# Optimization experiments

Hardware: AMD Instinct MI355X
Metric: run time of the kernel (lower is better)

## Reference

```python
import jax, jax.numpy as jnp
import numpy as np

N = 100000            # number of nodes
E = 1600000           # number of edges (avg degree 16)
D = 32                # embedding dim
MASK_DEPTH = 3        # cfg.mask_depth
PATH_PROB = 0.5       # cfg.path_prob
NUM_MASK_CAND = 1024  # cfg.num_mask_cand
EPS_NORM = 1e-12      # F.normalize eps


def setup_inputs() -> dict:
    key = jax.random.key(0)
    k1, k2 = jax.random.split(key)
    edge_index = jax.random.randint(k1, (2, E), 0, N)  # [2, E] (row, col) COO indices
    adj_values = jnp.ones((E,), dtype=jnp.float32)     # sparse values (binary adjacency)
    embeds = jax.random.normal(k2, (N, D), dtype=jnp.float32)
    return {"edge_index": edge_index, "adj_values": adj_values, "embeds": embeds}


def _spmm(rows, cols, vals, x):
    # out[i] = sum_{e: rows[e]==i} vals[e] * x[cols[e]]  -- irregular gather + scatter-add
    return jax.ops.segment_sum(x[cols] * vals[:, None], rows, num_segments=N)


def _l2_normalize(x):
    n = jnp.sqrt(jnp.sum(x * x, axis=-1, keepdims=True))
    return x / jnp.maximum(n, EPS_NORM)


def reference(edge_index, adj_values, embeds):
    rows, cols = edge_index[0], edge_index[1]
    vals = adj_values

    # order = row-sums of sparse adj, shape [N, 1]
    order = jax.ops.segment_sum(vals, rows, num_segments=N)[:, None]

    fst_emb = _spmm(rows, cols, vals, embeds) - embeds
    fst_num = order
    emb = [fst_emb]
    num = [fst_num]

    drop_key = jax.random.key(42)
    for i in range(MASK_DEPTH):
        # sparse_dropout with keep prob path_prob**(i+1); zeroing values == dropping edges in spmm
        keep_prob = PATH_PROB ** (i + 1)
        u = jax.random.uniform(jax.random.fold_in(drop_key, i), (E,))
        keep = jnp.floor(u + keep_prob)  # 1.0 with prob keep_prob, else 0.0
        vals = vals * keep               # dropout compounds across iterations

        emb.append(_spmm(rows, cols, vals, emb[-1]) - emb[-1] - order * emb[-1])
        num.append(_spmm(rows, cols, vals, num[-1]) - num[-1] - order)
        order = jax.ops.segment_sum(vals, rows, num_segments=N)[:, None]

    subgraph_embeds = sum(emb) / (sum(num) + 1e-8)
    subgraph_embeds = _l2_normalize(subgraph_embeds)
    embeds_n = _l2_normalize(embeds)

    scores = jnp.sum(subgraph_embeds * embeds_n, axis=-1)  # [N]
    # Gumbel noise: -log(-log(U))
    u = jax.random.uniform(jax.random.key(7), (N,))
    scores = scores + (-jnp.log(-jnp.log(u)))

    _, candidates = jax.lax.top_k(scores, NUM_MASK_CAND)
    return scores, candidates
```

## Files before the change

kernel.cpp:

```cpp
#include <hip/hip_runtime.h>
#include <stdint.h>
#include <stddef.h>

#define NN 100000
#define NE 1600000
#define DD 32
#define NCAND 1024
#define HSIZE 65536
#define SORTN 4096
#define NBUK ((NN + 255) / 256)
#define EPB 4096
#define BCAP 5120
#define BCAPL 4608
#define CHK 5

#define CAP1 832000
#define CAP2 432000
#define CAP3 240000

__host__ __device__ inline void tf2x32(uint32_t k0, uint32_t k1, uint32_t x0, uint32_t x1,
                                       uint32_t& o0, uint32_t& o1) {
  uint32_t ks2 = k0 ^ k1 ^ 0x1BD11BDAu;
  uint32_t v0 = x0 + k0, v1 = x1 + k1;
#define TFR(r) { v0 += v1; v1 = (v1 << (r)) | (v1 >> (32 - (r))); v1 ^= v0; }
  TFR(13) TFR(15) TFR(26) TFR(6)   v0 += k1;  v1 += ks2 + 1u;
  TFR(17) TFR(29) TFR(16) TFR(24)  v0 += ks2; v1 += k0 + 2u;
  TFR(13) TFR(15) TFR(26) TFR(6)   v0 += k0;  v1 += k1 + 3u;
  TFR(17) TFR(29) TFR(16) TFR(24)  v0 += k1;  v1 += ks2 + 4u;
  TFR(13) TFR(15) TFR(26) TFR(6)   v0 += ks2; v1 += k0 + 5u;
#undef TFR
  o0 = v0; o1 = v1;
}

__device__ __forceinline__ uint32_t jax_bits32(uint32_t k0, uint32_t k1, uint32_t i) {
  uint32_t o0, o1;
  tf2x32(k0, k1, 0u, i, o0, o1);
  return o0 ^ o1;
}

__device__ __forceinline__ float bits_to_uniform(uint32_t b) {
  return __fsub_rn(__uint_as_float((b >> 9) | 0x3f800000u), 1.0f);
}

__device__ __forceinline__ float pw32c(float4 c0, float4 c1, float4 c2, float4 c3,
                                       float4 c4, float4 c5, float4 c6, float4 c7) {
  float r0 = __fadd_rn(__fadd_rn(__fadd_rn(c0.x, c2.x), c4.x), c6.x);
  float r1 = __fadd_rn(__fadd_rn(__fadd_rn(c0.y, c2.y), c4.y), c6.y);
  float r2 = __fadd_rn(__fadd_rn(__fadd_rn(c0.z, c2.z), c4.z), c6.z);
  float r3 = __fadd_rn(__fadd_rn(__fadd_rn(c0.w, c2.w), c4.w), c6.w);
  float r4 = __fadd_rn(__fadd_rn(__fadd_rn(c1.x, c3.x), c5.x), c7.x);
  float r5 = __fadd_rn(__fadd_rn(__fadd_rn(c1.y, c3.y), c5.y), c7.y);
  float r6 = __fadd_rn(__fadd_rn(__fadd_rn(c1.z, c3.z), c5.z), c7.z);
  float r7 = __fadd_rn(__fadd_rn(__fadd_rn(c1.w, c3.w), c5.w), c7.w);
  float a01 = __fadd_rn(r0, r1), a23 = __fadd_rn(r2, r3);
  float a45 = __fadd_rn(r4, r5), a67 = __fadd_rn(r6, r7);
  return __fadd_rn(__fadd_rn(a01, a23), __fadd_rn(a45, a67));
}

__device__ __forceinline__ float4 f4div1(float4 a, float d) {
  return make_float4(__fdiv_rn(a.x, d), __fdiv_rn(a.y, d),
                     __fdiv_rn(a.z, d), __fdiv_rn(a.w, d));
}
__device__ __forceinline__ float4 f4sq(float4 a) {
  return make_float4(__fmul_rn(a.x, a.x), __fmul_rn(a.y, a.y),
                     __fmul_rn(a.z, a.z), __fmul_rn(a.w, a.w));
}
__device__ __forceinline__ float4 f4dd(float4 s, float n1, float4 e, float n2) {
  return make_float4(__fmul_rn(__fdiv_rn(s.x, n1), __fdiv_rn(e.x, n2)),
                     __fmul_rn(__fdiv_rn(s.y, n1), __fdiv_rn(e.y, n2)),
                     __fmul_rn(__fdiv_rn(s.z, n1), __fdiv_rn(e.z, n2)),
                     __fmul_rn(__fdiv_rn(s.w, n1), __fdiv_rn(e.w, n2)));
}

__global__ __launch_bounds__(1024) void kA2_bin(
    const int* __restrict__ rows, const int* __restrict__ cols,
    const float* __restrict__ adj,
    uint32_t k00, uint32_t k01, uint32_t k10, uint32_t k11,
    uint32_t k20, uint32_t k21,
    int* __restrict__ bucketCursor, int4* __restrict__ pkBin,
    int* __restrict__ bucketCntS) {
  __shared__ int hist[NBUK];
  __shared__ int base[NBUK];
  __shared__ int h1[NBUK];
  __shared__ int h2[NBUK];
  __shared__ int h3[NBUK];
  __shared__ uint8_t lvs[EPB];
  __shared__ uint16_t rank16[EPB];
  int tid = threadIdx.x;
  for (int i = tid; i < NBUK; i += 1024) { hist[i] = 0; h1[i] = 0; h2[i] = 0; h3[i] = 0; }
  __syncthreads();
  int e0 = blockIdx.x * EPB;
#pragma unroll
  for (int k = 0; k < 4; ++k) {
    int e = e0 + k * 1024 + tid;
    int lv = 0;
    if (e < NE) {
      float u0 = bits_to_uniform(jax_bits32(k00, k01, (uint32_t)e));
      float u1 = bits_to_uniform(jax_bits32(k10, k11, (uint32_t)e));
      float u2 = bits_to_uniform(jax_bits32(k20, k21, (uint32_t)e));
      float kp0 = floorf(__fadd_rn(u0, 0.5f));
      float kp1 = floorf(__fadd_rn(u1, 0.25f));
      float kp2 = floorf(__fadd_rn(u2, 0.125f));
      if (kp0 != 0.0f) { lv = 1; if (kp1 != 0.0f) { lv = 2; if (kp2 != 0.0f) lv = 3; } }
      int b = rows[e] >> 8;
      rank16[k * 1024 + tid] = (uint16_t)atomicAdd(&hist[b], 1);
      if (lv >= 1) {
        atomicAdd(&h1[b], 1);
        if (lv >= 2) {
          atomicAdd(&h2[b], 1);
          if (lv >= 3) atomicAdd(&h3[b], 1);
        }
      }
    }
    lvs[k * 1024 + tid] = (uint8_t)lv;
  }
  __syncthreads();
  for (int i = tid; i < NBUK; i += 1024) {
    int h = hist[i];
    base[i] = (h > 0) ? atomicAdd(&bucketCursor[i], h) : 0;
    if (h1[i]) atomicAdd(&bucketCntS[i], h1[i]);
    if (h2[i]) atomicAdd(&bucketCntS[NBUK + i], h2[i]);
    if (h3[i]) atomicAdd(&bucketCntS[2 * NBUK + i], h3[i]);
  }
  __syncthreads();
#pragma unroll
  for (int k = 0; k < 4; ++k) {
    int e = e0 + k * 1024 + tid;
    if (e < NE) {
      int r = rows[e];
      int b = r >> 8;
      int lv = (int)lvs[k * 1024 + tid];
      int pos = base[b] + (int)rank16[k * 1024 + tid];
      if (pos < BCAP)
        pkBin[(size_t)b * BCAP + pos] =
            make_int4(cols[e], __float_as_int(adj[e]), (e << 2) | lv, r);
    }
  }
}

__global__ __launch_bounds__(512) void k_scanBS(const int* __restrict__ bucketCursor,
                                                const int* __restrict__ bucketCntS,
                                                int* __restrict__ bucketBaseS) {
  __shared__ int sb[512];
  int a = blockIdx.x;
  const int* c = (a == 0) ? bucketCursor : (bucketCntS + (size_t)(a - 1) * NBUK);
  int* o = bucketBaseS + (size_t)a * (NBUK + 1);
  int tid = threadIdx.x;
  int v = (tid < NBUK) ? c[tid] : 0;
  sb[tid] = v;
  __syncthreads();
  for (int off = 1; off < 512; off <<= 1) {
    int x = (tid >= off) ? sb[tid - off] : 0;
    __syncthreads();
    sb[tid] += x;
    __syncthreads();
  }
  if (tid < NBUK) o[tid] = sb[tid] - v;
  if (tid == NBUK - 1) o[NBUK] = sb[tid];
}

__global__ __launch_bounds__(1024) void kB_emit(
    const int* __restrict__ bucketBaseS, const int4* __restrict__ pkBin,
    int* __restrict__ rpAll,
    int2* __restrict__ pk0, int2* __restrict__ pk1,
    int2* __restrict__ pk2, int2* __restrict__ pk3,
    float* __restrict__ order0, float* __restrict__ order1, float* __restrict__ order2) {
  __shared__ unsigned long long cnt64[256];
  __shared__ unsigned long long scan64[1024];
  __shared__ int start0[256];
  __shared__ int cur[256];
  __shared__ uint32_t keyF[BCAPL];
  __shared__ uint32_t keyG[BCAPL];
  __shared__ uint16_t origG[BCAPL];
  int b = blockIdx.x, tid = threadIdx.x;
  int bB0 = bucketBaseS[b];
  int n = bucketBaseS[b + 1] - bB0;
  if (n > BCAPL) n = BCAPL;
  size_t sRead = (size_t)b * BCAP;
  const int* pkI = (const int*)pkBin;
  const int2* pkZW = (const int2*)pkBin;
  int r0 = b << 8;
  int nr = NN - r0; if (nr > 256) nr = 256;
  int bB1 = bucketBaseS[(NBUK + 1) + b];
  int bB2 = bucketBaseS[2 * (NBUK + 1) + b];
  int bB3 = bucketBaseS[3 * (NBUK + 1) + b];
  if (tid < 256) { cnt64[tid] = 0ull; cur[tid] = 0; }
  __syncthreads();
  for (int i = tid; i < n; i += 1024) {
    int2 zw = pkZW[2 * (sRead + (size_t)i) + 1];
    int lr = zw.y - r0;
    int lv = zw.x & 3;
    keyF[i] = ((uint32_t)lr << 23) | (uint32_t)zw.x;
    unsigned long long add = 1ull;
    if (lv >= 1) add |= 1ull << 16;
    if (lv >= 2) add |= 1ull << 32;
    if (lv >= 3) add |= 1ull << 48;
    atomicAdd(&cnt64[lr], add);
  }
  __syncthreads();
  unsigned long long own = (tid < 256) ? cnt64[tid] : 0ull;
  if (tid < 256) scan64[tid] = own;
  __syncthreads();
  for (int off = 1; off < 256; off <<= 1) {
    unsigned long long v = (tid < 256 && tid >= off) ? scan64[tid - off] : 0ull;
    __syncthreads();
    if (tid < 256) scan64[tid] += v;
    __syncthreads();
  }
  if (tid < 256) {
    unsigned long long ex = scan64[tid] - own;
    start0[tid] = (int)(ex & 0xFFFFull);
    if (tid < nr) {
      rpAll[r0 + tid] = bB0 + (int)(ex & 0xFFFFull);
      rpAll[(NN + 1) + r0 + tid] = bB1 + (int)((ex >> 16) & 0xFFFFull);
      rpAll[2 * (NN + 1) + r0 + tid] = bB2 + (int)((ex >> 32) & 0xFFFFull);
      rpAll[3 * (NN + 1) + r0 + tid] = bB3 + (int)((ex >> 48) & 0xFFFFull);
    }
  }
  if (b == NBUK - 1 && tid == 0) {
    rpAll[NN] = bucketBaseS[NBUK];
    rpAll[(NN + 1) + NN] = bucketBaseS[(NBUK + 1) + NBUK];
    rpAll[2 * (NN + 1) + NN] = bucketBaseS[2 * (NBUK + 1) + NBUK];
    rpAll[3 * (NN + 1) + NN] = bucketBaseS[3 * (NBUK + 1) + NBUK];
  }
  __syncthreads();
  for (int i = tid; i < n; i += 1024) {
    uint32_t k = keyF[i];
    int lr = (int)(k >> 23);
    int slot = start0[lr] + atomicAdd(&cur[lr], 1);
    origG[slot] = (uint16_t)i;
    keyG[slot] = k;
  }
  __syncthreads();
  int C2 = (n + 1023) >> 10;
  {
    int lo2 = tid * C2, hi2 = lo2 + C2;
    if (lo2 > n) lo2 = n;
    if (hi2 > n) hi2 = n;
    uint16_t vals[CHK];
    uint16_t pos[CHK];
    uint32_t keys[CHK];
#pragma unroll
    for (int q = 0; q < CHK; ++q) {
      int i = lo2 + q;
      if (i < hi2) {
        uint32_t ki = keyG[i];
        int lr = (int)(ki >> 23);
        int st = start0[lr];
        int d = (int)(cnt64[lr] & 0xFFFFull);
        int rank = 0;
        for (int j = 0; j < d; ++j) rank += (keyG[st + j] < ki) ? 1 : 0;
        vals[q] = origG[i];
        keys[q] = ki;
        pos[q] = (uint16_t)(st + rank);
      }
    }
    __syncthreads();
#pragma unroll
    for (int q = 0; q < CHK; ++q) {
      int i = lo2 + q;
      if (i < hi2) { origG[pos[q]] = vals[q]; keyG[pos[q]] = keys[q]; }
    }
  }
  __syncthreads();
  uint32_t* adjS = keyF;
  {
    uint32_t av[CHK];
#pragma unroll
    for (int q = 0; q < CHK; ++q) {
      int i = tid + q * 1024;
      if (i < n) av[q] = (uint32_t)pkI[4 * (sRead + (size_t)origG[i]) + 1];
    }
#pragma unroll
    for (int q = 0; q < CHK; ++q) {
      int i = tid + q * 1024;
      if (i < n) adjS[i] = av[q];
    }
  }
  __syncthreads();
  if (tid < nr) {
    int d = (int)(cnt64[tid] & 0xFFFFull);
    int st = start0[tid];
    float o0 = 0.0f, o1v = 0.0f, o2v = 0.0f;
    for (int i = 0; i < d; ++i) {
      int lv = (int)(keyG[st + i] & 3u);
      float a = __uint_as_float(adjS[st + i]);
      o0 = __fadd_rn(o0, a);
      if (lv >= 1) { o1v = __fadd_rn(o1v, a); if (lv >= 2) o2v = __fadd_rn(o2v, a); }
    }
    order0[r0 + tid] = o0; order1[r0 + tid] = o1v; order2[r0 + tid] = o2v;
  }
  int lo = tid * C2, hi = lo + C2;
  if (lo > n) lo = n;
  if (hi > n) hi = n;
  int c1 = 0, c2 = 0, c3 = 0;
  for (int i = lo; i < hi; ++i) {
    int lv = (int)(keyG[i] & 3u);
    c1 += (lv >= 1); c2 += (lv >= 2); c3 += (lv >= 3);
  }
  unsigned long long mine = (unsigned long long)c1 |
                            ((unsigned long long)c2 << 16) |
                            ((unsigned long long)c3 << 32);
  scan64[tid] = mine;
  __syncthreads();
  for (int off = 1; off < 1024; off <<= 1) {
    unsigned long long v = (tid >= off) ? scan64[tid - off] : 0ull;
    __syncthreads();
    scan64[tid] += v;
    __syncthreads();
  }
  unsigned long long ex = scan64[tid] - mine;
  int o1 = bB1 + (int)(ex & 0xFFFFull);
  int o2 = bB2 + (int)((ex >> 16) & 0xFFFFull);
  int o3 = bB3 + (int)((ex >> 32) & 0xFFFFull);
  {
    int colr[CHK];
#pragma unroll
    for (int q = 0; q < CHK; ++q) {
      int i = lo + q;
      if (i < hi) colr[q] = pkI[4 * (sRead + (size_t)origG[i])];
    }
#pragma unroll
    for (int q = 0; q < CHK; ++q) {
      int i = lo + q;
      if (i < hi) {
        int lv = (int)(keyG[i] & 3u);
        int2 pkv = make_int2(colr[q], (int)adjS[i]);
        pk0[bB0 + i] = pkv;
        if (lv >= 1) {
          pk1[o1++] = pkv;
          if (lv >= 2) {
            pk2[o2++] = pkv;
            if (lv >= 3) pk3[o3++] = pkv;
          }
        }
      }
    }
  }
}


__global__ void k_emb0(const int* __restrict__ rp, const int2* __restrict__ pk,
                       const float* __restrict__ embeds, float* __restrict__ e0) {
  int tid = blockIdx.x * blockDim.x + threadIdx.x;
  int r = tid >> 5, d = tid & 31;
  if (r >= NN) return;
  int s = rp[r], t = rp[r + 1];
  float acc = 0.0f;
  for (int base = s; base < t; base += 32) {
    int idx = base + d;
    int2 p = (idx < t) ? pk[idx] : make_int2(0, 0);
    int m = t - base; if (m > 32) m = 32;
    for (int j = 0; j < m; j += 8) {
      int cc[8], aa[8];
      float xx[8];
#pragma unroll
      for (int q = 0; q < 8; ++q) {
        cc[q] = __shfl(p.x, j + q, 32);
        aa[q] = __shfl(p.y, j + q, 32);
      }
#pragma unroll
      for (int q = 0; q < 8; ++q) xx[q] = embeds[(size_t)cc[q] * DD + d];
#pragma unroll
      for (int q = 0; q < 8; ++q)
        acc = __fadd_rn(acc, __fmul_rn(__int_as_float(aa[q]), xx[q]));
    }
  }
  e0[(size_t)r * DD + d] = __fsub_rn(acc, embeds[(size_t)r * DD + d]);
}

__global__ void k_emb_step(const int* __restrict__ rp, const int2* __restrict__ pk,
                           const float* __restrict__ ord, const float* __restrict__ ecur,
                           float* __restrict__ enext, float* __restrict__ esum,
                           const float* __restrict__ ncur, float* __restrict__ nnext,
                           float* __restrict__ nsum, int mode) {
  int tid = blockIdx.x * blockDim.x + threadIdx.x;
  int r = tid >> 5, d = tid & 31;
  if (r >= NN) return;
  int s = rp[r], t = rp[r + 1];
  float acc = 0.0f, accn = 0.0f;
  for (int base = s; base < t; base += 32) {
    int idx = base + d;
    int2 p = (idx < t) ? pk[idx] : make_int2(0, 0);
    int m = t - base; if (m > 32) m = 32;
    for (int j = 0; j < m; j += 8) {
      int cc[8], aa[8];
      float xx[8], nn[8];
#pragma unroll
      for (int q = 0; q < 8; ++q) {
        cc[q] = __shfl(p.x, j + q, 32);
        aa[q] = __shfl(p.y, j + q, 32);
      }
#pragma unroll
      for (int q = 0; q < 8; ++q) {
        xx[q] = ecur[(size_t)cc[q] * DD + d];
        nn[q] = ncur[cc[q]];
      }
#pragma unroll
      for (int q = 0; q < 8; ++q) {
        float av = __int_as_float(aa[q]);
        acc = __fadd_rn(acc, __fmul_rn(av, xx[q]));
        accn = __fadd_rn(accn, __fmul_rn(av, nn[q]));
      }
    }
  }
  float ordv = ord[r];
  size_t idx = (size_t)r * DD + d;
  float ec = ecur[idx];
  float o = __fsub_rn(__fsub_rn(acc, ec), __fmul_rn(ordv, ec));
  if (mode != 3) enext[idx] = o;
  if (mode == 1) esum[idx] = __fadd_rn(ec, o);
  else esum[idx] = __fadd_rn(esum[idx], o);
  if (d == 0) {
    float nc = ncur[r];
    float on = __fsub_rn(__fsub_rn(accn, nc), ordv);
    if (mode != 3) nnext[r] = on;
    if (mode == 1) nsum[r] = __fadd_rn(nc, on);
    else nsum[r] = __fadd_rn(nsum[r], on);
  }
}

__global__ __launch_bounds__(256) void k_score(
    const float* __restrict__ embeds, const float* __restrict__ emb_sum,
    const float* __restrict__ num_sum, uint32_t gk0, uint32_t gk1,
    float* __restrict__ out_scores) {
  __shared__ float sm[256 * 33];
  int t = threadIdx.x;
  int b = blockIdx.x;
  int f4base = b * 2048;
  const float4* gS = (const float4*)emb_sum;
  const float4* gE = (const float4*)embeds;
#pragma unroll
  for (int k = 0; k < 8; ++k) {
    int loc = k * 256 + t;
    int g = f4base + loc;
    if (g < NN * 8) {
      int row = loc >> 3, c4 = loc & 7;
      float4 v = gS[g];
      float* d1 = &sm[row * 33 + c4 * 4];
      d1[0] = v.x; d1[1] = v.y; d1[2] = v.z; d1[3] = v.w;
    }
  }
  __syncthreads();
  int r = b * 256 + t;
  int rc = (r < NN) ? r : 0;
  float denom = __fadd_rn(num_sum[rc], 1e-8f);
  const float* rs = &sm[t * 33];
  float4 s0 = f4div1(make_float4(rs[0], rs[1], rs[2], rs[3]), denom);
  float4 s1 = f4div1(make_float4(rs[4], rs[5], rs[6], rs[7]), denom);
  float4 s2 = f4div1(make_float4(rs[8], rs[9], rs[10], rs[11]), denom);
  float4 s3 = f4div1(make_float4(rs[12], rs[13], rs[14], rs[15]), denom);
  float4 s4 = f4div1(make_float4(rs[16], rs[17], rs[18], rs[19]), denom);
  float4 s5 = f4div1(make_float4(rs[20], rs[21], rs[22], rs[23]), denom);
  float4 s6 = f4div1(make_float4(rs[24], rs[25], rs[26], rs[27]), denom);
  float4 s7 = f4div1(make_float4(rs[28], rs[29], rs[30], rs[31]), denom);
  float n1 = fmaxf(__fsqrt_rn(pw32c(f4sq(s0), f4sq(s1), f4sq(s2), f4sq(s3),
                                    f4sq(s4), f4sq(s5), f4sq(s6), f4sq(s7))), 1e-12f);
  __syncthreads();
#pragma unroll
  for (int k = 0; k < 8; ++k) {
    int loc = k * 256 + t;
    int g = f4base + loc;
    if (g < NN * 8) {
      int row = loc >> 3, c4 = loc & 7;
      float4 w = gE[g];
      float* d2 = &sm[row * 33 + c4 * 4];
      d2[0] = w.x; d2[1] = w.y; d2[2] = w.z; d2[3] = w.w;
    }
  }
  __syncthreads();
  float4 m0 = make_float4(rs[0], rs[1], rs[2], rs[3]);
  float4 m1 = make_float4(rs[4], rs[5], rs[6], rs[7]);
  float4 m2 = make_float4(rs[8], rs[9], rs[10], rs[11]);
  float4 m3 = make_float4(rs[12], rs[13], rs[14], rs[15]);
  float4 m4 = make_float4(rs[16], rs[17], rs[18], rs[19]);
  float4 m5 = make_float4(rs[20], rs[21], rs[22], rs[23]);
  float4 m6 = make_float4(rs[24], rs[25], rs[26], rs[27]);
  float4 m7 = make_float4(rs[28], rs[29], rs[30], rs[31]);
  float n2 = fmaxf(__fsqrt_rn(pw32c(f4sq(m0), f4sq(m1), f4sq(m2), f4sq(m3),
                                    f4sq(m4), f4sq(m5), f4sq(m6), f4sq(m7))), 1e-12f);
  float dot = pw32c(f4dd(s0, n1, m0, n2), f4dd(s1, n1, m1, n2),
                    f4dd(s2, n1, m2, n2), f4dd(s3, n1, m3, n2),
                    f4dd(s4, n1, m4, n2), f4dd(s5, n1, m5, n2),
                    f4dd(s6, n1, m6, n2), f4dd(s7, n1, m7, n2));
  float u = bits_to_uniform(jax_bits32(gk0, gk1, (uint32_t)rc));
  float l1 = (float)log((double)u);
  float w = -l1;
  float l2 = (float)log((double)w);
  float g = -l2;
  if (r < NN) out_scores[r] = __fadd_rn(dot, g);
}

__global__ __launch_bounds__(1024) void k_hist(const float* __restrict__ scores,
                                               int* __restrict__ hist) {
  __shared__ uint32_t hb[1024];
  __shared__ uint32_t hc[1024];
  int t = threadIdx.x;
  int r = blockIdx.x * 1024 + t;
  hb[t] = 0xFFFFFFFFu;
  hc[t] = 0u;
  __syncthreads();
  if (r < NN) {
    uint32_t kb = __float_as_uint(scores[r]);
    kb = (kb & 0x80000000u) ? ~kb : (kb | 0x80000000u);
    uint32_t key = kb >> 16;
    uint32_t slot = (key * 2654435761u) >> 22;
    for (;;) {
      uint32_t prev = atomicCAS(&hb[slot], 0xFFFFFFFFu, key);
      if (prev == 0xFFFFFFFFu || prev == key) { atomicAdd(&hc[slot], 1u); break; }
      slot = (slot + 1) & 1023u;
    }
  }
  __syncthreads();
  if (hb[t] != 0xFFFFFFFFu) atomicAdd(&hist[hb[t]], (int)hc[t]);
}

__global__ void k_cutoff(const int* __restrict__ hist, int* __restrict__ cutoff) {
  __shared__ int psum[1024];
  int t = threadIdx.x;
  int base = HSIZE - (t + 1) * 64;
  int own = 0;
  for (int i = 0; i < 64; ++i) own += hist[base + i];
  psum[t] = own;
  __syncthreads();
  for (int off = 1; off < 1024; off <<= 1) {
    int v = (t >= off) ? psum[t - off] : 0;
    __syncthreads();
    psum[t] += v;
    __syncthreads();
  }
  int incl = psum[t];
  int prev = incl - own;
  if (incl >= NCAND && prev < NCAND) {
    int c = prev;
    int b = HSIZE - t * 64 - 1;
    while (b >= base) {
      c += hist[b];
      if (c >= NCAND) break;
      --b;
    }
    *cutoff = b;
  }
}

__global__ void k_collect(const float* __restrict__ scores, const int* __restrict__ cutoff,
                          unsigned long long* __restrict__ buf, int* __restrict__ cnt2) {
  int r = blockIdx.x * blockDim.x + threadIdx.x;
  if (r >= NN) return;
  uint32_t kb = __float_as_uint(scores[r]);
  kb = (kb & 0x80000000u) ? ~kb : (kb | 0x80000000u);
  if ((int)(kb >> 16) >= *cutoff) {
    int p = atomicAdd(cnt2, 1);
    if (p < SORTN)
      buf[p] = ((unsigned long long)kb << 32) | (uint32_t)(~(uint32_t)r);
  }
}

__global__ __launch_bounds__(256) void k_rank(const unsigned long long* __restrict__ buf,
                                              const int* __restrict__ cnt2,
                                              float* __restrict__ out_cand) {
  __shared__ unsigned long long s[SORTN];
  int m = *cnt2;
  if (m > SORTN) m = SORTN;
  if (blockIdx.x * 256 >= m) return;
  for (int i = threadIdx.x; i < m; i += 256) s[i] = buf[i];
  __syncthreads();
  int i = blockIdx.x * 256 + threadIdx.x;
  if (i >= m) return;
  unsigned long long mine = s[i];
  int rank = 0;
  int j = 0;
  for (; j + 8 <= m; j += 8) {
#pragma unroll
    for (int q = 0; q < 8; ++q) rank += (s[j + q] > mine) ? 1 : 0;
  }
  for (; j < m; ++j) rank += (s[j] > mine) ? 1 : 0;
  if (rank < NCAND) {
    uint32_t idx = ~((uint32_t)(mine & 0xffffffffull));
    out_cand[rank] = (float)idx;
  }
}

extern "C" void kernel_launch(void* const* d_in, const int* in_sizes, int n_in,
                              void* d_out, int out_size, void* d_ws, size_t ws_size,
                              hipStream_t stream) {
  const int* rows = (const int*)d_in[0];
  const int* cols = rows + NE;
  const float* adj = (const float*)d_in[1];
  const float* embeds = (const float*)d_in[2];
  float* out = (float*)d_out;

  char* p = (char*)d_ws;
  auto alloc = [&](size_t bytes) {
    char* q = p;
    p += (bytes + 255) & ~(size_t)255;
    return q;
  };
  size_t zero_bytes = (size_t)(4 * NBUK + HSIZE + 8) * 4;
  char* zero_base = (char*)alloc(zero_bytes);
  int* bucketCursor = (int*)zero_base;
  int* bucketCntS = bucketCursor + NBUK;
  int* hist = bucketCntS + 3 * NBUK;
  int* cnt2 = hist + HSIZE;

  int* bucketBaseS = (int*)alloc((size_t)4 * (NBUK + 1) * 4);
  int* rpAll = (int*)alloc((size_t)4 * (NN + 1) * 4);
  size_t padBytes = (size_t)NBUK * BCAP * 16;
  char* unionAB = (char*)alloc(padBytes);
  int4* pkBin = (int4*)unionAB;
  float* embA = (float*)unionAB;
  float* embB = (float*)(unionAB + (size_t)NN * DD * 4);
  int2* pk0 = (int2*)alloc((size_t)NE * 8);
  int2* pk1 = (int2*)alloc((size_t)CAP1 * 8);
  int2* pk2 = (int2*)alloc((size_t)CAP2 * 8);
  int2* pk3 = (int2*)alloc((size_t)CAP3 * 8);
  float* embS = (float*)alloc((size_t)NN * DD * 4);
  float* order0 = (float*)alloc(NN * 4);
  float* order1 = (float*)alloc(NN * 4);
  float* order2 = (float*)alloc(NN * 4);
  float* num1 = (float*)alloc(NN * 4);
  float* num2 = (float*)alloc(NN * 4);
  float* numS = (float*)alloc(NN * 4);
  unsigned long long* buf = (unsigned long long*)alloc(SORTN * 8);

  uint32_t dk[3][2];
  for (int i = 0; i < 3; ++i) tf2x32(0u, 42u, 0u, (uint32_t)i, dk[i][0], dk[i][1]);

  hipMemsetAsync(zero_base, 0, zero_bytes, stream);

  int gE = (NE + EPB - 1) / EPB;
  kA2_bin<<<gE, 1024, 0, stream>>>(rows, cols, adj, dk[0][0], dk[0][1], dk[1][0], dk[1][1],
                                   dk[2][0], dk[2][1], bucketCursor, pkBin, bucketCntS);
  k_scanBS<<<4, 512, 0, stream>>>(bucketCursor, bucketCntS, bucketBaseS);
  kB_emit<<<NBUK, 1024, 0, stream>>>(bucketBaseS, pkBin, rpAll,
                                     pk0, pk1, pk2, pk3, order0, order1, order2);

  const int* rp0 = rpAll;
  const int* rp1 = rpAll + (NN + 1);
  const int* rp2 = rpAll + 2 * (NN + 1);
  const int* rp3 = rpAll + 3 * (NN + 1);

  int gEmb = (NN * 32 + 255) / 256;
  k_emb0<<<gEmb, 256, 0, stream>>>(rp0, pk0, embeds, embA);

  k_emb_step<<<gEmb, 256, 0, stream>>>(rp1, pk1, order0, embA, embB, embS,
                                       order0, num1, numS, 1);
  k_emb_step<<<gEmb, 256, 0, stream>>>(rp2, pk2, order1, embB, embA, embS,
                                       num1, num2, numS, 2);
  k_emb_step<<<gEmb, 256, 0, stream>>>(rp3, pk3, order2, embA, embB, embS,
                                       num2, num1, numS, 3);

  k_score<<<(NN + 255) / 256, 256, 0, stream>>>(embeds, embS, numS, 0u, 7u, out);
  k_hist<<<(NN + 1023) / 1024, 1024, 0, stream>>>(out, hist);
  k_cutoff<<<1, 1024, 0, stream>>>(hist, cnt2 + 1);
  k_collect<<<(NN + 255) / 256, 256, 0, stream>>>(out, cnt2 + 1, buf, cnt2);
  k_rank<<<(SORTN + 255) / 256, 256, 0, stream>>>(buf, cnt2, out + NN);
}
```

Measured before the change: 334.4 us.

## Pack bin counters into one atomic, locally sort edges, fuse histogram into score

The binning kernel now packs the total and the three per-level counts into one 32-bit shared atomic per bucket. It then scans those counts to place each edge at a bucket-sorted local position and writes the packed records in local bucket order, so global stores to the same bucket are contiguous. Separately, the score histogram is folded into k_score using a 512-slot hash, which removes one kernel launch and the reread of the scores. The costs are an extra intra-block scan, a second pass with more shared memory, and packed counters that overflow if any single block puts more than 1023 edges into one bucket.

```diff
diff --git a/kernel.cpp b/kernel.cpp
--- a/kernel.cpp
+++ b/kernel.cpp
@@ -79,21 +79,20 @@
     uint32_t k20, uint32_t k21,
     int* __restrict__ bucketCursor, int4* __restrict__ pkBin,
     int* __restrict__ bucketCntS) {
-  __shared__ int hist[NBUK];
+  __shared__ uint32_t histP[NBUK];
+  __shared__ int start0[512];
+  __shared__ int cur[NBUK];
   __shared__ int base[NBUK];
-  __shared__ int h1[NBUK];
-  __shared__ int h2[NBUK];
-  __shared__ int h3[NBUK];
   __shared__ uint8_t lvs[EPB];
-  __shared__ uint16_t rank16[EPB];
+  __shared__ uint32_t keyG2[EPB];
+  __shared__ uint16_t bukOf[EPB];
   int tid = threadIdx.x;
-  for (int i = tid; i < NBUK; i += 1024) { hist[i] = 0; h1[i] = 0; h2[i] = 0; h3[i] = 0; }
+  for (int i = tid; i < NBUK; i += 1024) { histP[i] = 0u; cur[i] = 0; }
   __syncthreads();
   int e0 = blockIdx.x * EPB;
 #pragma unroll
   for (int k = 0; k < 4; ++k) {
     int e = e0 + k * 1024 + tid;
-    int lv = 0;
     if (e < NE) {
       float u0 = bits_to_uniform(jax_bits32(k00, k01, (uint32_t)e));
       float u1 = bits_to_uniform(jax_bits32(k10, k11, (uint32_t)e));
@@ -101,26 +100,36 @@
       float kp0 = floorf(__fadd_rn(u0, 0.5f));
       float kp1 = floorf(__fadd_rn(u1, 0.25f));
       float kp2 = floorf(__fadd_rn(u2, 0.125f));
+      int lv = 0;
       if (kp0 != 0.0f) { lv = 1; if (kp1 != 0.0f) { lv = 2; if (kp2 != 0.0f) lv = 3; } }
       int b = rows[e] >> 8;
-      rank16[k * 1024 + tid] = (uint16_t)atomicAdd(&hist[b], 1);
-      if (lv >= 1) {
-        atomicAdd(&h1[b], 1);
-        if (lv >= 2) {
-          atomicAdd(&h2[b], 1);
-          if (lv >= 3) atomicAdd(&h3[b], 1);
-        }
-      }
-    }
-    lvs[k * 1024 + tid] = (uint8_t)lv;
-  }
-  __syncthreads();
-  for (int i = tid; i < NBUK; i += 1024) {
-    int h = hist[i];
-    base[i] = (h > 0) ? atomicAdd(&bucketCursor[i], h) : 0;
-    if (h1[i]) atomicAdd(&bucketCntS[i], h1[i]);
-    if (h2[i]) atomicAdd(&bucketCntS[NBUK + i], h2[i]);
-    if (h3[i]) atomicAdd(&bucketCntS[2 * NBUK + i], h3[i]);
+      uint32_t enc = 1u;
+      if (lv >= 1) { enc |= 1u << 10; if (lv >= 2) { enc |= 1u << 19; if (lv >= 3) enc |= 1u << 26; } }
+      atomicAdd(&histP[b], enc);
+      lvs[k * 1024 + tid] = (uint8_t)lv;
+    }
+  }
+  __syncthreads();
+  if (tid < 512) start0[tid] = (tid < NBUK) ? (int)(histP[tid] & 1023u) : 0;
+  __syncthreads();
+  for (int off = 1; off < 512; off <<= 1) {
+    int x = 0;
+    if (tid < 512 && tid >= off) x = start0[tid - off];
+    __syncthreads();
+    if (tid < 512) start0[tid] += x;
+    __syncthreads();
+  }
+  if (tid < NBUK) {
+    uint32_t h = histP[tid];
+    int h0 = (int)(h & 1023u);
+    start0[tid] -= h0;
+    base[tid] = (h0 > 0) ? atomicAdd(&bucketCursor[tid], h0) : 0;
+    int h1v = (int)((h >> 10) & 511u);
+    int h2v = (int)((h >> 19) & 127u);
+    int h3v = (int)((h >> 26) & 63u);
+    if (h1v) atomicAdd(&bucketCntS[tid], h1v);
+    if (h2v) atomicAdd(&bucketCntS[NBUK + tid], h2v);
+    if (h3v) atomicAdd(&bucketCntS[2 * NBUK + tid], h3v);
   }
   __syncthreads();
 #pragma unroll
@@ -130,11 +139,22 @@
       int r = rows[e];
       int b = r >> 8;
       int lv = (int)lvs[k * 1024 + tid];
-      int pos = base[b] + (int)rank16[k * 1024 + tid];
-      if (pos < BCAP)
-        pkBin[(size_t)b * BCAP + pos] =
-            make_int4(cols[e], __float_as_int(adj[e]), (e << 2) | lv, r);
-    }
+      int slot = start0[b] + atomicAdd(&cur[b], 1);
+      keyG2[slot] = ((uint32_t)(r & 255) << 23) | ((uint32_t)e << 2) | (uint32_t)lv;
+      bukOf[slot] = (uint16_t)b;
+    }
+  }
+  __syncthreads();
+  int n = NE - e0; if (n > EPB) n = EPB;
+  for (int i = tid; i < n; i += 1024) {
+    int b = (int)bukOf[i];
+    uint32_t kk = keyG2[i];
+    int eidlv = (int)(kk & 0x7FFFFFu);
+    int e = eidlv >> 2;
+    int pos = base[b] + (i - start0[b]);
+    if (pos < BCAP)
+      pkBin[(size_t)b * BCAP + pos] =
+          make_int4(cols[e], __float_as_int(adj[e]), eidlv, (b << 8) | (int)(kk >> 23));
   }
 }
 
@@ -423,10 +443,13 @@
 __global__ __launch_bounds__(256) void k_score(
     const float* __restrict__ embeds, const float* __restrict__ emb_sum,
     const float* __restrict__ num_sum, uint32_t gk0, uint32_t gk1,
-    float* __restrict__ out_scores) {
+    float* __restrict__ out_scores, int* __restrict__ hist) {
   __shared__ float sm[256 * 33];
+  __shared__ uint32_t hb[512];
+  __shared__ uint32_t hc[512];
   int t = threadIdx.x;
   int b = blockIdx.x;
+  for (int i = t; i < 512; i += 256) { hb[i] = 0xFFFFFFFFu; hc[i] = 0u; }
   int f4base = b * 2048;
   const float4* gS = (const float4*)emb_sum;
   const float4* gE = (const float4*)embeds;
@@ -488,31 +511,22 @@
   float w = -l1;
   float l2 = (float)log((double)w);
   float g = -l2;
-  if (r < NN) out_scores[r] = __fadd_rn(dot, g);
-}
-
-__global__ __launch_bounds__(1024) void k_hist(const float* __restrict__ scores,
-                                               int* __restrict__ hist) {
-  __shared__ uint32_t hb[1024];
-  __shared__ uint32_t hc[1024];
-  int t = threadIdx.x;
-  int r = blockIdx.x * 1024 + t;
-  hb[t] = 0xFFFFFFFFu;
-  hc[t] = 0u;
-  __syncthreads();
+  float score = __fadd_rn(dot, g);
   if (r < NN) {
-    uint32_t kb = __float_as_uint(scores[r]);
+    out_scores[r] = score;
+    uint32_t kb = __float_as_uint(score);
     kb = (kb & 0x80000000u) ? ~kb : (kb | 0x80000000u);
     uint32_t key = kb >> 16;
-    uint32_t slot = (key * 2654435761u) >> 22;
+    uint32_t slot = (key * 2654435761u) >> 23;
     for (;;) {
       uint32_t prev = atomicCAS(&hb[slot], 0xFFFFFFFFu, key);
       if (prev == 0xFFFFFFFFu || prev == key) { atomicAdd(&hc[slot], 1u); break; }
-      slot = (slot + 1) & 1023u;
-    }
-  }
-  __syncthreads();
-  if (hb[t] != 0xFFFFFFFFu) atomicAdd(&hist[hb[t]], (int)hc[t]);
+      slot = (slot + 1) & 511u;
+    }
+  }
+  __syncthreads();
+  for (int i = t; i < 512; i += 256)
+    if (hb[i] != 0xFFFFFFFFu) atomicAdd(&hist[hb[i]], (int)hc[i]);
 }
 
 __global__ void k_cutoff(const int* __restrict__ hist, int* __restrict__ cutoff) {
@@ -650,8 +664,7 @@
   k_emb_step<<<gEmb, 256, 0, stream>>>(rp3, pk3, order2, embA, embB, embS,
                                        num2, num1, numS, 3);
 
-  k_score<<<(NN + 255) / 256, 256, 0, stream>>>(embeds, embS, numS, 0u, 7u, out);
-  k_hist<<<(NN + 1023) / 1024, 1024, 0, stream>>>(out, hist);
+  k_score<<<(NN + 255) / 256, 256, 0, stream>>>(embeds, embS, numS, 0u, 7u, out, hist);
   k_cutoff<<<1, 1024, 0, stream>>>(hist, cnt2 + 1);
   k_collect<<<(NN + 255) / 256, 256, 0, stream>>>(out, cnt2 + 1, buf, cnt2);
   k_rank<<<(SORTN + 255) / 256, 256, 0, stream>>>(buf, cnt2, out + NN);
```

New measurement: 342.0 us. +2.3%, slower.
